# Performance work log

Measured on AMD Instinct MI355X. Metric: run time of the kernel, lower is better.

Reference implementation:

```python
import jax, jax.numpy as jnp
import numpy as np

B, D = 8192, 8          # batch, number of input features (= number of TT cores)
P = 10                  # poly_deg + 1 (basis width per feature)
R = 512                 # fixed TT rank
OUT = 64                # output dim (dims[0])
N_MID = D - 2           # middle cores
U_LO, U_HI = -0.1, 0.1  # uniform init range


def setup_inputs() -> dict:
    key = jax.random.key(0)
    kz, k0, km, kl = jax.random.split(key, 4)
    z = jax.random.normal(kz, (B, D), dtype=jnp.float32)
    G0 = jax.random.uniform(k0, (P, R), minval=U_LO, maxval=U_HI, dtype=jnp.float32)
    G_mid = jax.random.uniform(km, (N_MID, R, P, R), minval=U_LO, maxval=U_HI, dtype=jnp.float32)
    G_last = jax.random.uniform(kl, (R, P, OUT), minval=U_LO, maxval=U_HI, dtype=jnp.float32)
    return {"z": z, "G0": G0, "G_mid": G_mid, "G_last": G_last, "t": 0}


def _poly_basis(z, p):
    # Phi[i] = [z_i^0, ..., z_i^(p-1)]  -> stacked as [B, D, P]
    return z[:, :, None] ** jnp.arange(p, dtype=z.dtype)


def reference(z, G0, G_mid, G_last, t):
    phi = _poly_basis(z, G0.shape[0])                 # [B, D, P]
    # first core: tanh(G0)[j, r], Phi0[b, j] -> res[b, r]
    res = jnp.einsum('jr,bj->br', jnp.tanh(G0), phi[:, 0, :])
    # middle cores: res[b,i] . tanh(G)[i,j,k] . Phi[b,j] -> [b,k]
    for i in range(G_mid.shape[0]):
        tmp = jnp.einsum('bi,ijk->bjk', res, jnp.tanh(G_mid[i]))   # [B, P, R]
        res = jnp.einsum('bjk,bj->bk', tmp, phi[:, i + 1, :])      # [B, R]
    # last core -> output dim
    tmp = jnp.einsum('bi,ijl->bjl', res, jnp.tanh(G_last))         # [B, P, OUT]
    res = jnp.einsum('bjl,bj->bl', tmp, phi[:, -1, :])             # [B, OUT]
    return res
```

## Files before the change

### kernel.cpp

```cpp
#include <hip/hip_runtime.h>
#include <hip/hip_bf16.h>
#include <stdint.h>

#define BB   8192
#define DD   8
#define PP   10
#define RR   512
#define OUTD 64
#define KK   5120

typedef __bf16 bf16x8 __attribute__((ext_vector_type(8)));
typedef float  f32x4  __attribute__((ext_vector_type(4)));

__device__ __forceinline__ float poly_tanh(float x) {
    const float t = x * x;
    float p = fmaf(t, -0.05396825397f, 0.13333333333f);
    p = fmaf(t, p, -0.33333333333f);
    return fmaf(x * t, p, x);
}

template <int N>
__global__ __launch_bounds__(256) void frag_pack(
        const float* __restrict__ G, __hip_bfloat16* __restrict__ dst, int ldi) {
    constexpr int LOGN = (N == 512) ? 9 : 6;
    constexpr int PAD = 2;
    __shared__ __hip_bfloat16 sT[32 * (N + PAD)];
    const int kc = blockIdx.x, j = blockIdx.y, c = blockIdx.z;
    const float* Gp = G + (size_t)c * 512 * ldi;
    __hip_bfloat16* db = dst + (size_t)c * 5120 * N + (size_t)(j * 16 + kc) * 32 * N;
    #pragma unroll
    for (int e = 0; e < N / 32; ++e) {
        const int idx = (e * 256 + threadIdx.x) * 4;
        const int row = idx >> LOGN, col = idx & (N - 1);
        f32x4 v = *(const f32x4*)(Gp + (size_t)(kc * 32 + row) * ldi + (size_t)j * N + col);
        __hip_bfloat16* sp = sT + row * (N + PAD) + col;
        sp[0] = __float2bfloat16(poly_tanh(v.x));
        sp[1] = __float2bfloat16(poly_tanh(v.y));
        sp[2] = __float2bfloat16(poly_tanh(v.z));
        sp[3] = __float2bfloat16(poly_tanh(v.w));
    }
    __syncthreads();
    #pragma unroll
    for (int cc = 0; cc < N / 64; ++cc) {
        const int ch = cc * 256 + threadIdx.x;
        const int nt = ch >> 6, l = ch & 63;
        const int r0 = (l >> 4) * 8, cb = nt * 16 + (l & 15);
        union { __hip_bfloat16 h[8]; uint4 u; } pk;
        #pragma unroll
        for (int e = 0; e < 8; ++e) pk.h[e] = sT[(r0 + e) * (N + PAD) + cb];
        *(uint4*)(db + (size_t)ch * 8) = pk.u;
    }
}

__global__ __launch_bounds__(512) void tt_first(
        const float* __restrict__ z, const float* __restrict__ G0,
        __hip_bfloat16* __restrict__ res0) {
    const int r = threadIdx.x;
    const int b0 = blockIdx.x * 32;
    float tg[10];
    #pragma unroll
    for (int j = 0; j < 10; ++j) tg[j] = poly_tanh(G0[j * RR + r]);
    #pragma unroll 1
    for (int b = 0; b < 32; ++b) {
        const float z0 = z[(size_t)(b0 + b) * DD];
        float acc = tg[9];
        #pragma unroll
        for (int j = 8; j >= 0; --j) acc = acc * z0 + tg[j];
        res0[(size_t)(b0 + b) * RR + r] = __float2bfloat16(acc);
    }
}

template <bool LASTV, int NTOT, int SN, int MINW>
__global__ __launch_bounds__(256, MINW) void tt_gemm_ks(
        const __hip_bfloat16* __restrict__ resin,
        const __hip_bfloat16* __restrict__ tBf,
        void* __restrict__ outp,
        const float* __restrict__ z, int d) {
    __shared__ f32x4 red[2][4 * SN][64];

    const int tid  = threadIdx.x;
    const int lane = tid & 63;
    const int wave = tid >> 6;
    const int m0 = blockIdx.x * 64;
    const int nb = blockIdx.y;
    const int r16 = lane & 15, quad = lane >> 4;

    bf16x8 a[16];
    #pragma unroll
    for (int ms = 0; ms < 4; ++ms)
        #pragma unroll
        for (int kst = 0; kst < 4; ++kst)
            a[ms * 4 + kst] = *(const bf16x8*)(
                resin + (size_t)(m0 + ms * 16 + r16) * RR + wave * 128 + kst * 32 + quad * 8);

    float zr[16];
    #pragma unroll
    for (int ms = 0; ms < 4; ++ms)
        #pragma unroll
        for (int r = 0; r < 4; ++r)
            zr[ms * 4 + r] = z[(size_t)(m0 + ms * 16 + quad * 4 + r) * DD + d];

    f32x4 acc[4][SN];
    #pragma unroll
    for (int ms = 0; ms < 4; ++ms)
        #pragma unroll
        for (int sn = 0; sn < SN; ++sn) acc[ms][sn] = f32x4{0.f, 0.f, 0.f, 0.f};

    constexpr size_t SK = (size_t)NTOT * 512;
    constexpr size_t PJ = 16 * SK;
    const __hip_bfloat16* pB = tBf + (size_t)nb * SN * 512
                             + (size_t)wave * 4 * SK + (size_t)lane * 8;

    bf16x8 bv[4][SN];
    #pragma unroll
    for (int s = 0; s < 3; ++s)
        #pragma unroll
        for (int sn = 0; sn < SN; ++sn)
            bv[s][sn] = *(const bf16x8*)(pB + (size_t)9 * PJ + (size_t)s * SK + sn * 512);

#define MFMA_STEP(SLOT)                                                        \
    _Pragma("unroll")                                                          \
    for (int ms = 0; ms < 4; ++ms)                                             \
        _Pragma("unroll")                                                      \
        for (int sn = 0; sn < SN; ++sn)                                        \
            acc[ms][sn] = __builtin_amdgcn_mfma_f32_16x16x32_bf16(             \
                a[ms * 4 + SLOT], bv[SLOT][sn], acc[ms][sn], 0, 0, 0);

    #pragma unroll 1
    for (int p = 0; p < 10; ++p) {
        const int j = 9 - p;
        if (p) {
            #pragma unroll
            for (int ms = 0; ms < 4; ++ms)
                #pragma unroll
                for (int sn = 0; sn < SN; ++sn)
                    #pragma unroll
                    for (int r = 0; r < 4; ++r)
                        acc[ms][sn][r] *= zr[ms * 4 + r];
        }
        const size_t jb = (size_t)j * PJ;
        #pragma unroll
        for (int sn = 0; sn < SN; ++sn)
            bv[3][sn] = *(const bf16x8*)(pB + jb + (size_t)3 * SK + sn * 512);
        MFMA_STEP(0)
        if (p < 9) {
            #pragma unroll
            for (int sn = 0; sn < SN; ++sn)
                bv[0][sn] = *(const bf16x8*)(pB + jb - PJ + sn * 512);
        }
        MFMA_STEP(1)
        if (p < 9) {
            #pragma unroll
            for (int sn = 0; sn < SN; ++sn)
                bv[1][sn] = *(const bf16x8*)(pB + jb - PJ + SK + sn * 512);
        }
        MFMA_STEP(2)
        if (p < 9) {
            #pragma unroll
            for (int sn = 0; sn < SN; ++sn)
                bv[2][sn] = *(const bf16x8*)(pB + jb - PJ + 2 * SK + sn * 512);
        }
        MFMA_STEP(3)
    }
#undef MFMA_STEP

    if (wave & 1) {
        const int idx = wave >> 1;
        #pragma unroll
        for (int i = 0; i < 4 * SN; ++i) red[idx][i][lane] = acc[i / SN][i % SN];
    }
    __syncthreads();
    if (wave == 0) {
        #pragma unroll
        for (int i = 0; i < 4 * SN; ++i) acc[i / SN][i % SN] += red[0][i][lane];
    }
    if (wave == 2) {
        #pragma unroll
        for (int i = 0; i < 4 * SN; ++i) {
            f32x4 t = acc[i / SN][i % SN] + red[1][i][lane];
            red[1][i][lane] = t;
        }
    }
    __syncthreads();
    float* rc = (float*)&red[0][0][0];
    if (wave == 0) {
        #pragma unroll
        for (int i = 0; i < 4 * SN; ++i) acc[i / SN][i % SN] += red[1][i][lane];
        #pragma unroll
        for (int ms = 0; ms < 4; ++ms)
            #pragma unroll
            for (int sn = 0; sn < SN; ++sn)
                #pragma unroll
                for (int r = 0; r < 4; ++r)
                    rc[(ms * 16 + quad * 4 + r) * (SN * 16) + sn * 16 + r16] = acc[ms][sn][r];
    }
    __syncthreads();

    if (LASTV) {
        const int row = tid >> 2, cg = (tid & 3) * 16;
        float* o = (float*)outp;
        #pragma unroll
        for (int q = 0; q < 4; ++q)
            *(f32x4*)(o + (size_t)(m0 + row) * OUTD + cg + q * 4) =
                *(const f32x4*)(rc + row * 64 + cg + q * 4);
    } else {
        const int row = tid >> 2, cg = (tid & 3) * 8;
        __hip_bfloat16* o = (__hip_bfloat16*)outp;
        union { __hip_bfloat16 hh[8]; uint4 u; } pk;
        #pragma unroll
        for (int e = 0; e < 8; ++e)
            pk.hh[e] = __float2bfloat16(rc[row * (SN * 16) + cg + e]);
        *(uint4*)(o + (size_t)(m0 + row) * RR + nb * (SN * 16) + cg) = pk.u;
    }
}

extern "C" void kernel_launch(void* const* d_in, const int* in_sizes, int n_in,
                              void* d_out, int out_size, void* d_ws, size_t ws_size,
                              hipStream_t stream) {
    const float* z     = (const float*)d_in[0];
    const float* G0    = (const float*)d_in[1];
    const float* Gmid  = (const float*)d_in[2];
    const float* Glast = (const float*)d_in[3];
    float* out = (float*)d_out;

    char* ws = (char*)d_ws;
    __hip_bfloat16* resX   = (__hip_bfloat16*)ws;
    __hip_bfloat16* resY   = (__hip_bfloat16*)(ws + ((size_t)8 << 20));
    __hip_bfloat16* tBf    = (__hip_bfloat16*)(ws + ((size_t)16 << 20));
    __hip_bfloat16* tBlf   = (__hip_bfloat16*)(ws + ((size_t)48 << 20));

    frag_pack<512><<<dim3(16, 10, 6), 256, 0, stream>>>(Gmid,  tBf,  PP * RR);
    frag_pack<64> <<<dim3(16, 10, 1), 256, 0, stream>>>(Glast, tBlf, PP * OUTD);
    tt_first<<<dim3(BB / 32), 512, 0, stream>>>(z, G0, resX);

    __hip_bfloat16* rin = resX;
    __hip_bfloat16* rnext = resY;
    for (int c = 0; c < 6; ++c) {
        tt_gemm_ks<false, 32, 2, 3><<<dim3(BB / 64, RR / 32), 256, 0, stream>>>(
            rin, tBf + (size_t)c * RR * KK, rnext, z, c + 1);
        __hip_bfloat16* t = rin; rin = rnext; rnext = t;
    }
    tt_gemm_ks<true, 4, 4, 2><<<dim3(BB / 64, 1), 256, 0, stream>>>(
        rin, tBlf, out, z, 7);
}
```

Measured before the change: 404.8 us.

## Widen GEMM tiles to 64 columns and 128 rows per block

Middle-core GEMMs now run 512-thread blocks covering two 64-row M halves, each with four K-split waves computing 64 output columns (SN fixed at 4). Shared memory and the epilogue are reworked for the two halves. The aim is to reuse B fragments across more rows and cut per-block overhead. The cost is more accumulator and B registers per wave (occupancy hint of 2) and fewer blocks in the grid.

```diff
diff --git a/kernel.cpp b/kernel.cpp
--- a/kernel.cpp
+++ b/kernel.cpp
@@ -70,18 +70,21 @@
     }
 }
 
-template <bool LASTV, int NTOT, int SN, int MINW>
-__global__ __launch_bounds__(256, MINW) void tt_gemm_ks(
+template <bool LASTV, int NTOT, int WM>
+__global__ __launch_bounds__(WM * 256, 2) void tt_gemm_ks(
         const __hip_bfloat16* __restrict__ resin,
         const __hip_bfloat16* __restrict__ tBf,
         void* __restrict__ outp,
         const float* __restrict__ z, int d) {
-    __shared__ f32x4 red[2][4 * SN][64];
+    __shared__ f32x4 red[WM][2][16][64];
 
     const int tid  = threadIdx.x;
     const int lane = tid & 63;
     const int wave = tid >> 6;
-    const int m0 = blockIdx.x * 64;
+    const int mh = wave >> 2;
+    const int kw = wave & 3;
+    const int gm0 = blockIdx.x * (64 * WM);
+    const int mb  = gm0 + mh * 64;
     const int nb = blockIdx.y;
     const int r16 = lane & 15, quad = lane >> 4;
 
@@ -91,38 +94,38 @@
         #pragma unroll
         for (int kst = 0; kst < 4; ++kst)
             a[ms * 4 + kst] = *(const bf16x8*)(
-                resin + (size_t)(m0 + ms * 16 + r16) * RR + wave * 128 + kst * 32 + quad * 8);
+                resin + (size_t)(mb + ms * 16 + r16) * RR + kw * 128 + kst * 32 + quad * 8);
 
     float zr[16];
     #pragma unroll
     for (int ms = 0; ms < 4; ++ms)
         #pragma unroll
         for (int r = 0; r < 4; ++r)
-            zr[ms * 4 + r] = z[(size_t)(m0 + ms * 16 + quad * 4 + r) * DD + d];
-
-    f32x4 acc[4][SN];
+            zr[ms * 4 + r] = z[(size_t)(mb + ms * 16 + quad * 4 + r) * DD + d];
+
+    f32x4 acc[4][4];
     #pragma unroll
     for (int ms = 0; ms < 4; ++ms)
         #pragma unroll
-        for (int sn = 0; sn < SN; ++sn) acc[ms][sn] = f32x4{0.f, 0.f, 0.f, 0.f};
+        for (int sn = 0; sn < 4; ++sn) acc[ms][sn] = f32x4{0.f, 0.f, 0.f, 0.f};
 
     constexpr size_t SK = (size_t)NTOT * 512;
     constexpr size_t PJ = 16 * SK;
-    const __hip_bfloat16* pB = tBf + (size_t)nb * SN * 512
-                             + (size_t)wave * 4 * SK + (size_t)lane * 8;
-
-    bf16x8 bv[4][SN];
+    const __hip_bfloat16* pB = tBf + (size_t)nb * 4 * 512
+                             + (size_t)kw * 4 * SK + (size_t)lane * 8;
+
+    bf16x8 bv[4][4];
     #pragma unroll
     for (int s = 0; s < 3; ++s)
         #pragma unroll
-        for (int sn = 0; sn < SN; ++sn)
+        for (int sn = 0; sn < 4; ++sn)
             bv[s][sn] = *(const bf16x8*)(pB + (size_t)9 * PJ + (size_t)s * SK + sn * 512);
 
 #define MFMA_STEP(SLOT)                                                        \
     _Pragma("unroll")                                                          \
     for (int ms = 0; ms < 4; ++ms)                                             \
         _Pragma("unroll")                                                      \
-        for (int sn = 0; sn < SN; ++sn)                                        \
+        for (int sn = 0; sn < 4; ++sn)                                         \
             acc[ms][sn] = __builtin_amdgcn_mfma_f32_16x16x32_bf16(             \
                 a[ms * 4 + SLOT], bv[SLOT][sn], acc[ms][sn], 0, 0, 0);
 
@@ -133,84 +136,90 @@
             #pragma unroll
             for (int ms = 0; ms < 4; ++ms)
                 #pragma unroll
-                for (int sn = 0; sn < SN; ++sn)
+                for (int sn = 0; sn < 4; ++sn)
                     #pragma unroll
                     for (int r = 0; r < 4; ++r)
                         acc[ms][sn][r] *= zr[ms * 4 + r];
         }
         const size_t jb = (size_t)j * PJ;
         #pragma unroll
-        for (int sn = 0; sn < SN; ++sn)
+        for (int sn = 0; sn < 4; ++sn)
             bv[3][sn] = *(const bf16x8*)(pB + jb + (size_t)3 * SK + sn * 512);
         MFMA_STEP(0)
         if (p < 9) {
             #pragma unroll
-            for (int sn = 0; sn < SN; ++sn)
+            for (int sn = 0; sn < 4; ++sn)
                 bv[0][sn] = *(const bf16x8*)(pB + jb - PJ + sn * 512);
         }
         MFMA_STEP(1)
         if (p < 9) {
             #pragma unroll
-            for (int sn = 0; sn < SN; ++sn)
+            for (int sn = 0; sn < 4; ++sn)
                 bv[1][sn] = *(const bf16x8*)(pB + jb - PJ + SK + sn * 512);
         }
         MFMA_STEP(2)
         if (p < 9) {
             #pragma unroll
-            for (int sn = 0; sn < SN; ++sn)
+            for (int sn = 0; sn < 4; ++sn)
                 bv[2][sn] = *(const bf16x8*)(pB + jb - PJ + 2 * SK + sn * 512);
         }
         MFMA_STEP(3)
     }
 #undef MFMA_STEP
 
-    if (wave & 1) {
-        const int idx = wave >> 1;
-        #pragma unroll
-        for (int i = 0; i < 4 * SN; ++i) red[idx][i][lane] = acc[i / SN][i % SN];
-    }
-    __syncthreads();
-    if (wave == 0) {
-        #pragma unroll
-        for (int i = 0; i < 4 * SN; ++i) acc[i / SN][i % SN] += red[0][i][lane];
-    }
-    if (wave == 2) {
-        #pragma unroll
-        for (int i = 0; i < 4 * SN; ++i) {
-            f32x4 t = acc[i / SN][i % SN] + red[1][i][lane];
-            red[1][i][lane] = t;
-        }
-    }
-    __syncthreads();
-    float* rc = (float*)&red[0][0][0];
-    if (wave == 0) {
-        #pragma unroll
-        for (int i = 0; i < 4 * SN; ++i) acc[i / SN][i % SN] += red[1][i][lane];
+    if (kw & 1) {
+        const int idx = kw >> 1;
+        #pragma unroll
+        for (int i = 0; i < 16; ++i) red[mh][idx][i][lane] = acc[i >> 2][i & 3];
+    }
+    __syncthreads();
+    if (kw == 0) {
+        #pragma unroll
+        for (int i = 0; i < 16; ++i) acc[i >> 2][i & 3] += red[mh][0][i][lane];
+    }
+    if (kw == 2) {
+        #pragma unroll
+        for (int i = 0; i < 16; ++i) {
+            f32x4 t = acc[i >> 2][i & 3] + red[mh][1][i][lane];
+            red[mh][1][i][lane] = t;
+        }
+    }
+    __syncthreads();
+    if (kw == 0) {
+        float* rcw = (float*)&red[mh][0][0][0];
+        #pragma unroll
+        for (int i = 0; i < 16; ++i) acc[i >> 2][i & 3] += red[mh][1][i][lane];
         #pragma unroll
         for (int ms = 0; ms < 4; ++ms)
             #pragma unroll
-            for (int sn = 0; sn < SN; ++sn)
+            for (int sn = 0; sn < 4; ++sn)
                 #pragma unroll
                 for (int r = 0; r < 4; ++r)
-                    rc[(ms * 16 + quad * 4 + r) * (SN * 16) + sn * 16 + r16] = acc[ms][sn][r];
-    }
-    __syncthreads();
-
+                    rcw[(ms * 16 + quad * 4 + r) * 64 + sn * 16 + r16] = acc[ms][sn][r];
+    }
+    __syncthreads();
+
+    const int t = tid & 255;
+    const int mh2 = tid >> 8;
+    const float* rc = (const float*)&red[mh2][0][0][0];
+    const int row = t >> 2, cg = (t & 3) * 16;
     if (LASTV) {
-        const int row = tid >> 2, cg = (tid & 3) * 16;
         float* o = (float*)outp;
         #pragma unroll
         for (int q = 0; q < 4; ++q)
-            *(f32x4*)(o + (size_t)(m0 + row) * OUTD + cg + q * 4) =
+            *(f32x4*)(o + (size_t)(gm0 + row) * OUTD + cg + q * 4) =
                 *(const f32x4*)(rc + row * 64 + cg + q * 4);
     } else {
-        const int row = tid >> 2, cg = (tid & 3) * 8;
         __hip_bfloat16* o = (__hip_bfloat16*)outp;
-        union { __hip_bfloat16 hh[8]; uint4 u; } pk;
-        #pragma unroll
-        for (int e = 0; e < 8; ++e)
-            pk.hh[e] = __float2bfloat16(rc[row * (SN * 16) + cg + e]);
-        *(uint4*)(o + (size_t)(m0 + row) * RR + nb * (SN * 16) + cg) = pk.u;
+        const size_t grow = (size_t)(gm0 + mh2 * 64 + row);
+        #pragma unroll
+        for (int h = 0; h < 2; ++h) {
+            union { __hip_bfloat16 hh[8]; uint4 u; } pk;
+            #pragma unroll
+            for (int e = 0; e < 8; ++e)
+                pk.hh[e] = __float2bfloat16(rc[row * 64 + cg + h * 8 + e]);
+            *(uint4*)(o + grow * RR + nb * 64 + cg + h * 8) = pk.u;
+        }
     }
 }
 
@@ -236,10 +245,10 @@
     __hip_bfloat16* rin = resX;
     __hip_bfloat16* rnext = resY;
     for (int c = 0; c < 6; ++c) {
-        tt_gemm_ks<false, 32, 2, 3><<<dim3(BB / 64, RR / 32), 256, 0, stream>>>(
+        tt_gemm_ks<false, 32, 2><<<dim3(BB / 128, RR / 64), 512, 0, stream>>>(
             rin, tBf + (size_t)c * RR * KK, rnext, z, c + 1);
         __hip_bfloat16* t = rin; rin = rnext; rnext = t;
     }
-    tt_gemm_ks<true, 4, 4, 2><<<dim3(BB / 64, 1), 256, 0, stream>>>(
+    tt_gemm_ks<true, 4, 1><<<dim3(BB / 64, 1), 256, 0, stream>>>(
         rin, tBlf, out, z, 7);
 }
```

After: 399.4 us. Within noise of the previous version (-1.3%).
